# Kernel optimization log

Measured on AMD Instinct MI355X. Metric: run time of the kernel, lower is better.

The kernel has to match this reference:

```python
import jax, jax.numpy as jnp
import numpy as np

N, IN, HID, OUT = 8192, 128, 256, 64

def setup_inputs() -> dict:
    key = jax.random.key(0)
    k = jax.random.split(key, 6)
    s1 = 1.0 / np.sqrt(IN)
    s2 = 1.0 / np.sqrt(HID)
    return {
        "x": jax.random.normal(k[0], (N, IN), dtype=jnp.float32),
        "adj": jax.random.uniform(k[1], (N, N), dtype=jnp.float32),
        "W1": jax.random.uniform(k[2], (HID, IN), jnp.float32, -s1, s1),
        "b1": jax.random.uniform(k[3], (HID,), jnp.float32, -s1, s1),
        "W2": jax.random.uniform(k[4], (OUT, HID), jnp.float32, -s2, s2),
        "b2": jax.random.uniform(k[5], (OUT,), jnp.float32, -s2, s2),
    }

def reference(x, adj, W1, b1, W2, b2):
    # deg_inv_sqrt @ adj @ deg_inv_sqrt == row/col elementwise scaling (same math,
    # without materializing diagonal matrices or doing O(N^3) GEMMs)
    deg = adj.sum(axis=1)
    d = 1.0 / jnp.sqrt(deg + 1e-8)  # [N]
    norm_adj = d[:, None] * adj * d[None, :]  # [N, N]
    h = jax.nn.relu((norm_adj @ x) @ W1.T + b1)  # [N, HID]
    return (norm_adj @ h) @ W2.T + b2  # [N, OUT]
```

## Files before the change

kernel.cpp:

```cpp
#include <hip/hip_runtime.h>
#include <hip/hip_bf16.h>

typedef float f32x4 __attribute__((ext_vector_type(4)));
typedef __bf16 bf16x8 __attribute__((ext_vector_type(8)));
typedef __bf16 bf16x4 __attribute__((ext_vector_type(4)));

#define N_NODES 8192
#define IN_F    128
#define HID_F   256
#define OUT_F   64
#define SPLIT1  8
#define SPLIT2  16

__device__ __forceinline__ void dma16(const void* g, void* l) {
  __builtin_amdgcn_global_load_lds(
      (const __attribute__((address_space(1))) void*)g,
      (__attribute__((address_space(3))) void*)(uint32_t)(uintptr_t)l, 16, 0, 0);
}

__global__ __launch_bounds__(256) void k_degcvt(const float* __restrict__ adj,
                                                __bf16* __restrict__ adjb,
                                                float* __restrict__ d) {
  const int row = blockIdx.x;
  const int t = threadIdx.x;
  const f32x4* p = (const f32x4*)(adj + (size_t)row * N_NODES);
  bf16x4* q = (bf16x4*)(adjb + (size_t)row * N_NODES);
  float s = 0.f;
#pragma unroll
  for (int i = 0; i < N_NODES / (256 * 4); ++i) {
    f32x4 v = p[i * 256 + t];
    s += v[0] + v[1] + v[2] + v[3];
    bf16x4 o = {(__bf16)v[0], (__bf16)v[1], (__bf16)v[2], (__bf16)v[3]};
    q[i * 256 + t] = o;
  }
#pragma unroll
  for (int off = 32; off > 0; off >>= 1) s += __shfl_down(s, off);
  __shared__ float red[4];
  if ((t & 63) == 0) red[t >> 6] = s;
  __syncthreads();
  if (t == 0) d[row] = rsqrtf(red[0] + red[1] + red[2] + red[3] + 1e-8f);
}

__global__ __launch_bounds__(256) void k_bt1(const float* __restrict__ x,
                                             const float* __restrict__ d,
                                             __bf16* __restrict__ Bt1) {
  __shared__ __bf16 tile[IN_F][64 + 2];
  const int t = threadIdx.x;
  const int j0 = blockIdx.x * 64;
#pragma unroll
  for (int rep = 0; rep < 32; ++rep) {
    int e = rep * 256 + t;
    int j = e >> 7, c = e & 127;
    tile[c][j] = (__bf16)(x[(size_t)(j0 + j) * IN_F + c] * d[j0 + j]);
  }
  __syncthreads();
#pragma unroll
  for (int rep = 0; rep < 32; ++rep) {
    int e = rep * 256 + t;
    int c = e >> 6, jj = e & 63;
    Bt1[(size_t)c * N_NODES + j0 + jj] = tile[c][jj];
  }
}

__device__ inline bf16x8 load_frag(const float* p) {
  f32x4 a = *(const f32x4*)p;
  f32x4 b = *(const f32x4*)(p + 4);
  bf16x8 o = {(__bf16)a[0], (__bf16)a[1], (__bf16)a[2], (__bf16)a[3],
              (__bf16)b[0], (__bf16)b[1], (__bf16)b[2], (__bf16)b[3]};
  return o;
}

template <int WGM, int WGN, int KC>
__global__ __launch_bounds__(256, 2) void k_gemm_dma(
    const __bf16* __restrict__ A, const __bf16* __restrict__ Bt,
    float* __restrict__ P) {
  constexpr int BM = WGM * 64, BN = WGN * 64;
  constexpr int ANI = BM / 64, BNI = BN / 64;
  constexpr int ABYTES = BM * 64;
  constexpr int STAGE = (BM + BN) * 64;
  constexpr int NIT = KC / 32;

  __shared__ __align__(16) char sm[2 * STAGE];

  const int t = threadIdx.x;
  const int w = t >> 6, lane = t & 63;
  const int r = lane & 15, q = lane >> 4;
  const int wm = (WGN == 1) ? w : (w >> 1);
  const int wn = (WGN == 1) ? 0 : (w & 1);
  const int m0 = blockIdx.x * BM;
  const int ks = blockIdx.y;
  const int k0 = ks * KC;

  const int n_ = t >> 2;
  const int csw = (t & 3) ^ ((t >> 3) & 3);
  const __bf16* a_src[ANI];
  const __bf16* b_src[BNI];
#pragma unroll
  for (int kk = 0; kk < ANI; ++kk)
    a_src[kk] = A + (size_t)(m0 + n_ + 64 * kk) * N_NODES + k0 + csw * 8;
#pragma unroll
  for (int kk = 0; kk < BNI; ++kk)
    b_src[kk] = Bt + (size_t)(n_ + 64 * kk) * N_NODES + k0 + csw * 8;

  int offA[4], offB[4];
#pragma unroll
  for (int tm = 0; tm < 4; ++tm) {
    const int row = wm * 64 + tm * 16 + r;
    offA[tm] = row * 64 + ((q ^ ((row >> 1) & 3)) << 4);
  }
#pragma unroll
  for (int ct = 0; ct < 4; ++ct) {
    const int row = wn * 64 + ct * 16 + r;
    offB[ct] = ABYTES + row * 64 + ((q ^ ((row >> 1) & 3)) << 4);
  }

  f32x4 acc[4][4];
#pragma unroll
  for (int tm = 0; tm < 4; ++tm)
#pragma unroll
    for (int ct = 0; ct < 4; ++ct) acc[tm][ct] = (f32x4){0.f, 0.f, 0.f, 0.f};

  {
    char* sb = sm;
#pragma unroll
    for (int kk = 0; kk < ANI; ++kk) {
      dma16(a_src[kk], sb + kk * 4096 + (w << 10));
      a_src[kk] += 32;
    }
#pragma unroll
    for (int kk = 0; kk < BNI; ++kk) {
      dma16(b_src[kk], sb + ABYTES + kk * 4096 + (w << 10));
      b_src[kk] += 32;
    }
  }
  __syncthreads();

#pragma unroll 2
  for (int it = 0; it < NIT; ++it) {
    char* cb = sm + (it & 1) * STAGE;
    if (it + 1 < NIT) {
      char* nb = sm + ((it + 1) & 1) * STAGE;
#pragma unroll
      for (int kk = 0; kk < ANI; ++kk) {
        dma16(a_src[kk], nb + kk * 4096 + (w << 10));
        a_src[kk] += 32;
      }
#pragma unroll
      for (int kk = 0; kk < BNI; ++kk) {
        dma16(b_src[kk], nb + ABYTES + kk * 4096 + (w << 10));
        b_src[kk] += 32;
      }
    }
    bf16x8 af[4], bfr[4];
#pragma unroll
    for (int tm = 0; tm < 4; ++tm) af[tm] = *(const bf16x8*)(cb + offA[tm]);
#pragma unroll
    for (int ct = 0; ct < 4; ++ct) bfr[ct] = *(const bf16x8*)(cb + offB[ct]);
#pragma unroll
    for (int tm = 0; tm < 4; ++tm)
#pragma unroll
      for (int ct = 0; ct < 4; ++ct)
        acc[tm][ct] = __builtin_amdgcn_mfma_f32_16x16x32_bf16(
            af[tm], bfr[ct], acc[tm][ct], 0, 0, 0);
    __syncthreads();
  }

  float* pout =
      P + ((size_t)ks * N_NODES + m0 + wm * 64 + q * 4) * BN + wn * 64 + r;
#pragma unroll
  for (int tm = 0; tm < 4; ++tm)
#pragma unroll
    for (int ct = 0; ct < 4; ++ct)
#pragma unroll
      for (int i = 0; i < 4; ++i)
        pout[(size_t)(tm * 16 + i) * BN + ct * 16] = acc[tm][ct][i];
}

__global__ __launch_bounds__(256) void k_red_mlp(const float* __restrict__ P1,
                                                 const float* __restrict__ dvec,
                                                 const float* __restrict__ W1,
                                                 const float* __restrict__ b1,
                                                 const float* __restrict__ W2,
                                                 __bf16* __restrict__ Bt2) {
  __shared__ __align__(16) float y[16][IN_F + 4];
  __shared__ __align__(16) __bf16 h[16][HID_F + 8];
  __shared__ __align__(16) float gl[OUT_F][20];
  __shared__ float dl[16];
  const int t = threadIdx.x;
  const int lane = t & 63;
  const int w = t >> 6;
  const int r = lane & 15, q = lane >> 4;
  const int j0 = blockIdx.x * 16;

  if (t < 16) dl[t] = dvec[j0 + t];
  const size_t plane4 = (size_t)N_NODES * IN_F / 4;
  for (int e = t; e < 16 * IN_F / 4; e += 256) {
    const int jj = e >> 5, c4 = e & 31;
    const size_t base = (size_t)(j0 + jj) * (IN_F / 4) + c4;
    f32x4 v = (f32x4){0.f, 0.f, 0.f, 0.f};
#pragma unroll
    for (int s = 0; s < SPLIT1; ++s) v += ((const f32x4*)P1)[base + s * plane4];
    const float dj = dvec[j0 + jj];
    v *= dj;
    *(f32x4*)&y[jj][c4 * 4] = v;
  }
  __syncthreads();

  f32x4 hacc[4];
#pragma unroll
  for (int tt = 0; tt < 4; ++tt) hacc[tt] = (f32x4){0.f, 0.f, 0.f, 0.f};
#pragma unroll
  for (int kt = 0; kt < 4; ++kt) {
    bf16x8 afr = load_frag((const float*)&y[r][kt * 32 + q * 8]);
#pragma unroll
    for (int tt = 0; tt < 4; ++tt) {
      const int col = w * 64 + tt * 16 + r;
      bf16x8 bfr = load_frag(W1 + (size_t)col * IN_F + kt * 32 + q * 8);
      hacc[tt] = __builtin_amdgcn_mfma_f32_16x16x32_bf16(afr, bfr, hacc[tt], 0, 0, 0);
    }
  }
#pragma unroll
  for (int tt = 0; tt < 4; ++tt) {
    const int col = w * 64 + tt * 16 + r;
    const float bias = b1[col];
#pragma unroll
    for (int i = 0; i < 4; ++i)
      h[q * 4 + i][col] = (__bf16)fmaxf(hacc[tt][i] + bias, 0.f);
  }
  __syncthreads();

  f32x4 gacc = (f32x4){0.f, 0.f, 0.f, 0.f};
  const int o = w * 16 + r;
#pragma unroll
  for (int kt = 0; kt < 8; ++kt) {
    bf16x8 afr = *(const bf16x8*)&h[r][kt * 32 + q * 8];
    bf16x8 bfr = load_frag(W2 + (size_t)o * HID_F + kt * 32 + q * 8);
    gacc = __builtin_amdgcn_mfma_f32_16x16x32_bf16(afr, bfr, gacc, 0, 0, 0);
  }
#pragma unroll
  for (int i = 0; i < 4; ++i) gl[o][q * 4 + i] = gacc[i];
  __syncthreads();

  const int oo = t >> 2, r0 = (t & 3) * 4;
  bf16x4 ov;
#pragma unroll
  for (int rr = 0; rr < 4; ++rr) ov[rr] = (__bf16)(gl[oo][r0 + rr] * dl[r0 + rr]);
  *(bf16x4*)(Bt2 + (size_t)oo * N_NODES + j0 + r0) = ov;
}

__global__ __launch_bounds__(256) void k_out(const float* __restrict__ P2,
                                             const float* __restrict__ dvec,
                                             const float* __restrict__ b2,
                                             float* __restrict__ out) {
  const int idx = blockIdx.x * 256 + threadIdx.x;
  const int j = idx >> 4, o4 = idx & 15;
  const size_t plane4 = (size_t)N_NODES * OUT_F / 4;
  f32x4 s = (f32x4){0.f, 0.f, 0.f, 0.f};
#pragma unroll
  for (int sp = 0; sp < SPLIT2; ++sp) s += ((const f32x4*)P2)[idx + sp * plane4];
  s *= dvec[j];
  s += ((const f32x4*)b2)[o4];
  ((f32x4*)out)[idx] = s;
}

extern "C" void kernel_launch(void* const* d_in, const int* in_sizes, int n_in,
                              void* d_out, int out_size, void* d_ws,
                              size_t ws_size, hipStream_t stream) {
  const float* x   = (const float*)d_in[0];
  const float* adj = (const float*)d_in[1];
  const float* W1  = (const float*)d_in[2];
  const float* b1  = (const float*)d_in[3];
  const float* W2  = (const float*)d_in[4];
  const float* b2  = (const float*)d_in[5];
  float* out = (float*)d_out;
  char* ws = (char*)d_ws;

  size_t off = 0;
  __bf16* adjb = (__bf16*)(ws + off); off += (size_t)N_NODES * N_NODES * 2;
  float*  dvec = (float*)(ws + off);  off += (size_t)N_NODES * 4;
  __bf16* Bt1  = (__bf16*)(ws + off); off += (size_t)IN_F * N_NODES * 2;
  float*  P1   = (float*)(ws + off);  off += (size_t)SPLIT1 * N_NODES * IN_F * 4;
  __bf16* Bt2  = (__bf16*)(ws + off); off += (size_t)OUT_F * N_NODES * 2;
  float*  P2   = (float*)(ws + off);

  hipLaunchKernelGGL(k_degcvt, dim3(N_NODES), dim3(256), 0, stream, adj, adjb, dvec);
  hipLaunchKernelGGL(k_bt1, dim3(N_NODES / 64), dim3(256), 0, stream, x, dvec, Bt1);
  hipLaunchKernelGGL((k_gemm_dma<2, 2, N_NODES / SPLIT1>),
                     dim3(N_NODES / 128, SPLIT1), dim3(256), 0, stream,
                     adjb, Bt1, P1);
  hipLaunchKernelGGL(k_red_mlp, dim3(N_NODES / 16), dim3(256), 0, stream, P1,
                     dvec, W1, b1, W2, Bt2);
  hipLaunchKernelGGL((k_gemm_dma<4, 1, N_NODES / SPLIT2>),
                     dim3(N_NODES / 256, SPLIT2), dim3(256), 0, stream,
                     adjb, Bt2, P2);
  hipLaunchKernelGGL(k_out, dim3((N_NODES * OUT_F / 4) / 256), dim3(256), 0,
                     stream, P2, dvec, b2, out);
}
```

Baseline: 485.9 us.

## Deepen GEMM LDS pipeline to four stages with explicit vmcnt waits

Replaces the double-buffered global-to-LDS DMA loop in the bf16 MFMA GEMM with a four-buffer ring that keeps three K-steps of loads in flight. Each step waits on a precise s_waitcnt vmcnt count plus a raw s_barrier, instead of a full __syncthreads drain. A tail of three specialised iterations shrinks the wait count as prefetching stops. The aim is to hide global-load latency behind MFMA work. In exchange it quadruples the per-block LDS footprint, which can reduce occupancy, and it depends on hand-placed waits staying consistent with the number of issued DMAs.

```diff
diff --git a/kernel.cpp b/kernel.cpp
--- a/kernel.cpp
+++ b/kernel.cpp
@@ -16,6 +16,17 @@
   __builtin_amdgcn_global_load_lds(
       (const __attribute__((address_space(1))) void*)g,
       (__attribute__((address_space(3))) void*)(uint32_t)(uintptr_t)l, 16, 0, 0);
+}
+
+template <int K> __device__ __forceinline__ void wait_vmcnt() {
+  if constexpr (K == 0)       asm volatile("s_waitcnt vmcnt(0)" ::: "memory");
+  else if constexpr (K == 4)  asm volatile("s_waitcnt vmcnt(4)" ::: "memory");
+  else if constexpr (K == 5)  asm volatile("s_waitcnt vmcnt(5)" ::: "memory");
+  else if constexpr (K == 8)  asm volatile("s_waitcnt vmcnt(8)" ::: "memory");
+  else if constexpr (K == 10) asm volatile("s_waitcnt vmcnt(10)" ::: "memory");
+  else if constexpr (K == 12) asm volatile("s_waitcnt vmcnt(12)" ::: "memory");
+  else if constexpr (K == 15) asm volatile("s_waitcnt vmcnt(15)" ::: "memory");
+  else static_assert(K == 0, "unsupported vmcnt literal");
 }
 
 __global__ __launch_bounds__(256) void k_degcvt(const float* __restrict__ adj,
@@ -68,6 +79,54 @@
   bf16x8 o = {(__bf16)a[0], (__bf16)a[1], (__bf16)a[2], (__bf16)a[3],
               (__bf16)b[0], (__bf16)b[1], (__bf16)b[2], (__bf16)b[3]};
   return o;
+}
+
+template <int WGM, int WGN, int KC, int KWAIT>
+__device__ __forceinline__ void g_iter(char* sm, int t, int w,
+                                       const __bf16* (&a_src)[WGM],
+                                       const __bf16* (&b_src)[WGN],
+                                       const int (&offA)[4],
+                                       const int (&offB)[4],
+                                       f32x4 (&acc)[4][4]) {
+  constexpr int BM = WGM * 64, BN = WGN * 64;
+  constexpr int ABYTES = BM * 64;
+  constexpr int STAGE = (BM + BN) * 64;
+  constexpr int NIT = KC / 32;
+
+  if (t + 3 < NIT) {
+    char* nb = sm + ((t + 3) & 3) * STAGE;
+#pragma unroll
+    for (int kk = 0; kk < WGM; ++kk) {
+      dma16(a_src[kk], nb + kk * 4096 + (w << 10));
+      a_src[kk] += 32;
+    }
+#pragma unroll
+    for (int kk = 0; kk < WGN; ++kk) {
+      dma16(b_src[kk], nb + ABYTES + kk * 4096 + (w << 10));
+      b_src[kk] += 32;
+    }
+  }
+  __builtin_amdgcn_sched_barrier(0);
+  wait_vmcnt<KWAIT>();
+  asm volatile("s_barrier" ::: "memory");
+  __builtin_amdgcn_sched_barrier(0);
+
+  const char* cb = sm + (t & 3) * STAGE;
+  bf16x8 af[4], bfr[4];
+#pragma unroll
+  for (int tm = 0; tm < 4; ++tm) af[tm] = *(const bf16x8*)(cb + offA[tm]);
+#pragma unroll
+  for (int ct = 0; ct < 4; ++ct) bfr[ct] = *(const bf16x8*)(cb + offB[ct]);
+#pragma unroll
+  for (int tm = 0; tm < 4; ++tm)
+#pragma unroll
+    for (int ct = 0; ct < 4; ++ct)
+      acc[tm][ct] = __builtin_amdgcn_mfma_f32_16x16x32_bf16(
+          af[tm], bfr[ct], acc[tm][ct], 0, 0, 0);
+
+  __builtin_amdgcn_sched_barrier(0);
+  asm volatile("s_waitcnt lgkmcnt(0)" ::: "memory");
+  asm volatile("s_barrier" ::: "memory");
 }
 
 template <int WGM, int WGN, int KC>
@@ -79,8 +138,10 @@
   constexpr int ABYTES = BM * 64;
   constexpr int STAGE = (BM + BN) * 64;
   constexpr int NIT = KC / 32;
-
-  __shared__ __align__(16) char sm[2 * STAGE];
+  constexpr int L = ANI + BNI;
+  static_assert(NIT > 3, "pipeline needs >3 K-steps");
+
+  __shared__ __align__(16) char sm[4 * STAGE];
 
   const int t = threadIdx.x;
   const int w = t >> 6, lane = t & 63;
@@ -120,8 +181,9 @@
 #pragma unroll
     for (int ct = 0; ct < 4; ++ct) acc[tm][ct] = (f32x4){0.f, 0.f, 0.f, 0.f};
 
-  {
-    char* sb = sm;
+#pragma unroll
+  for (int s = 0; s < 3; ++s) {
+    char* sb = sm + s * STAGE;
 #pragma unroll
     for (int kk = 0; kk < ANI; ++kk) {
       dma16(a_src[kk], sb + kk * 4096 + (w << 10));
@@ -133,37 +195,12 @@
       b_src[kk] += 32;
     }
   }
-  __syncthreads();
-
-#pragma unroll 2
-  for (int it = 0; it < NIT; ++it) {
-    char* cb = sm + (it & 1) * STAGE;
-    if (it + 1 < NIT) {
-      char* nb = sm + ((it + 1) & 1) * STAGE;
-#pragma unroll
-      for (int kk = 0; kk < ANI; ++kk) {
-        dma16(a_src[kk], nb + kk * 4096 + (w << 10));
-        a_src[kk] += 32;
-      }
-#pragma unroll
-      for (int kk = 0; kk < BNI; ++kk) {
-        dma16(b_src[kk], nb + ABYTES + kk * 4096 + (w << 10));
-        b_src[kk] += 32;
-      }
-    }
-    bf16x8 af[4], bfr[4];
-#pragma unroll
-    for (int tm = 0; tm < 4; ++tm) af[tm] = *(const bf16x8*)(cb + offA[tm]);
-#pragma unroll
-    for (int ct = 0; ct < 4; ++ct) bfr[ct] = *(const bf16x8*)(cb + offB[ct]);
-#pragma unroll
-    for (int tm = 0; tm < 4; ++tm)
-#pragma unroll
-      for (int ct = 0; ct < 4; ++ct)
-        acc[tm][ct] = __builtin_amdgcn_mfma_f32_16x16x32_bf16(
-            af[tm], bfr[ct], acc[tm][ct], 0, 0, 0);
-    __syncthreads();
-  }
+
+  for (int it = 0; it < NIT - 3; ++it)
+    g_iter<WGM, WGN, KC, 3 * L>(sm, it, w, a_src, b_src, offA, offB, acc);
+  g_iter<WGM, WGN, KC, 2 * L>(sm, NIT - 3, w, a_src, b_src, offA, offB, acc);
+  g_iter<WGM, WGN, KC, L>(sm, NIT - 2, w, a_src, b_src, offA, offB, acc);
+  g_iter<WGM, WGN, KC, 0>(sm, NIT - 1, w, a_src, b_src, offA, offB, acc);
 
   float* pout =
       P + ((size_t)ks * N_NODES + m0 + wm * 64 + q * 4) * BN + wn * 64 + r;
```

Result: no change. 489.2 us (+0.7%).
